# Performance work log

Hardware: AMD Instinct MI355X
Metric: run time of the kernel (lower is better)

Reference implementation:

```python
import jax, jax.numpy as jnp
import numpy as np

N = 4096       # num nodes == output_dim (delta is symmetrized NxN)
E = 65536      # num edges (avg degree 16)
IN_DIM = 128
H = 256        # hidden_dim (channels)
HEADS = 4


def setup_inputs():
    key = jax.random.key(0)
    ks = iter(jax.random.split(key, 40))
    def w(shape, s=0.05):
        return jax.random.normal(next(ks), shape, jnp.float32) * s
    inp = {}
    inp['x'] = jax.random.normal(next(ks), (N, IN_DIM), jnp.float32)
    inp['edge_index'] = jax.random.randint(next(ks), (2, E), 0, N)
    inp['pre_w'] = w((H, IN_DIM)); inp['pre_b'] = w((H,))
    for p in ('g1', 'g2'):
        inp[p + '_gcn_w'] = w((H, H)); inp[p + '_gcn_b'] = w((H,))
        inp[p + '_attn_in_w'] = w((3 * H, H)); inp[p + '_attn_in_b'] = w((3 * H,))
        inp[p + '_attn_out_w'] = w((H, H)); inp[p + '_attn_out_b'] = w((H,))
        inp[p + '_ffn_w1'] = w((2 * H, H)); inp[p + '_ffn_b1'] = w((2 * H,))
        inp[p + '_ffn_w2'] = w((H, 2 * H)); inp[p + '_ffn_b2'] = w((H,))
    inp['mlp_w1'] = w((H, H)); inp['mlp_b1'] = w((H,))
    inp['mlp_w2'] = w((N, H)); inp['mlp_b2'] = w((N,))
    return inp


def _gcn(x, src, dst, W, b):
    n = x.shape[0]
    x = x @ W.T
    loop = jnp.arange(n)
    s = jnp.concatenate([src, loop])
    d = jnp.concatenate([dst, loop])
    deg = jax.ops.segment_sum(jnp.ones(s.shape[0], x.dtype), d, num_segments=n)
    dinv = jnp.where(deg > 0, jax.lax.rsqrt(deg), 0.0)
    coef = (dinv[s] * dinv[d])[:, None]
    out = jax.ops.segment_sum(x[s] * coef, d, num_segments=n)
    return out + b


def _mha(h, in_w, in_b, out_w, out_b):
    # nn.MultiheadAttention self-attention over all N nodes (single dense graph)
    n, c = h.shape
    d = c // HEADS
    qkv = h @ in_w.T + in_b                      # [N, 3C]
    q, k, v = jnp.split(qkv, 3, axis=-1)
    q = q.reshape(n, HEADS, d).transpose(1, 0, 2) * (d ** -0.5)  # [h, n, d]
    k = k.reshape(n, HEADS, d).transpose(1, 0, 2)
    v = v.reshape(n, HEADS, d).transpose(1, 0, 2)
    a = jax.nn.softmax(jnp.einsum('hnd,hmd->hnm', q, k), axis=-1)
    o = jnp.einsum('hnm,hmd->hnd', a, v).transpose(1, 0, 2).reshape(n, c)
    return o @ out_w.T + out_b


def _gps(x, src, dst, gw, gb, iw, ib, ow, ob, w1, b1, w2, b2):
    # GPSConv, eval mode: dropout off, batch_norm (default running stats) = identity
    h1 = _gcn(x, src, dst, gw, gb) + x
    h2 = _mha(x, iw, ib, ow, ob) + x
    out = h1 + h2
    ff = jax.nn.relu(out @ w1.T + b1) @ w2.T + b2
    return out + ff


def reference(x, edge_index, pre_w, pre_b,
              g1_gcn_w, g1_gcn_b, g1_attn_in_w, g1_attn_in_b, g1_attn_out_w, g1_attn_out_b,
              g1_ffn_w1, g1_ffn_b1, g1_ffn_w2, g1_ffn_b2,
              g2_gcn_w, g2_gcn_b, g2_attn_in_w, g2_attn_in_b, g2_attn_out_w, g2_attn_out_b,
              g2_ffn_w1, g2_ffn_b1, g2_ffn_w2, g2_ffn_b2,
              mlp_w1, mlp_b1, mlp_w2, mlp_b2):
    src, dst = edge_index[0], edge_index[1]
    h = jax.nn.relu(x @ pre_w.T + pre_b)
    h = jax.nn.relu(_gps(h, src, dst, g1_gcn_w, g1_gcn_b, g1_attn_in_w, g1_attn_in_b,
                         g1_attn_out_w, g1_attn_out_b, g1_ffn_w1, g1_ffn_b1, g1_ffn_w2, g1_ffn_b2))
    h = jax.nn.relu(_gps(h, src, dst, g2_gcn_w, g2_gcn_b, g2_attn_in_w, g2_attn_in_b,
                         g2_attn_out_w, g2_attn_out_b, g2_ffn_w1, g2_ffn_b1, g2_ffn_w2, g2_ffn_b2))
    delta = jax.nn.relu(h @ mlp_w1.T + mlp_b1) @ mlp_w2.T + mlp_b2  # [N, N]
    return (delta + delta.T) * 0.5
```

## Files before the change

### kernel.cpp

```cpp
#include <hip/hip_runtime.h>

#define NN 4096
#define EE 65536
#define HC 256

typedef unsigned short ushort_t;
typedef __attribute__((ext_vector_type(8))) short bf16x8;
typedef __attribute__((ext_vector_type(4))) float f32x4;

__device__ __forceinline__ ushort_t f2bf(float f) {
    unsigned int u = __float_as_uint(f);
    unsigned int r = (u + 0x7fffu + ((u >> 16) & 1u)) >> 16;
    return (ushort_t)r;
}
__device__ __forceinline__ float bf2f(ushort_t u) {
    return __uint_as_float(((unsigned int)u) << 16);
}
__device__ __forceinline__ unsigned int pack2bf(float a, float b) {
    unsigned int ua = __float_as_uint(a) + 0x8000u;
    unsigned int ub = __float_as_uint(b) + 0x8000u;
    return __builtin_amdgcn_perm(ub, ua, 0x07060302u);
}

__global__ void deg_init_k(float* __restrict__ deg) {
    int i = blockIdx.x * 256 + threadIdx.x;
    deg[i] = 1.0f;
}
__global__ void deg_scatter_k(const int* __restrict__ dst, float* __restrict__ deg) {
    int e = blockIdx.x * 256 + threadIdx.x;
    atomicAdd(&deg[dst[e]], 1.0f);
}
__global__ void dinv_k(const float* __restrict__ deg, float* __restrict__ dinv) {
    int i = blockIdx.x * 256 + threadIdx.x;
    dinv[i] = rsqrtf(deg[i]);
}
__global__ __launch_bounds__(1024)
void scan_offsets_k(const float* __restrict__ deg, int* __restrict__ offs,
                    int* __restrict__ cursor) {
    __shared__ int part[1024];
    const int t = threadIdx.x;
    int c0 = (int)deg[t * 4 + 0] - 1;
    int c1 = (int)deg[t * 4 + 1] - 1;
    int c2 = (int)deg[t * 4 + 2] - 1;
    int c3 = (int)deg[t * 4 + 3] - 1;
    part[t] = c0 + c1 + c2 + c3;
    __syncthreads();
    for (int off = 1; off < 1024; off <<= 1) {
        int v = (t >= off) ? part[t - off] : 0;
        __syncthreads();
        part[t] += v;
        __syncthreads();
    }
    int base = (t == 0) ? 0 : part[t - 1];
    offs[t * 4 + 0] = base;
    offs[t * 4 + 1] = base + c0;
    offs[t * 4 + 2] = base + c0 + c1;
    offs[t * 4 + 3] = base + c0 + c1 + c2;
    cursor[t * 4 + 0] = base;
    cursor[t * 4 + 1] = base + c0;
    cursor[t * 4 + 2] = base + c0 + c1;
    cursor[t * 4 + 3] = base + c0 + c1 + c2;
    if (t == 1023) offs[4096] = part[1023];
}
__global__ void csr_fill_k(const int* __restrict__ src, const int* __restrict__ dst,
                           int* __restrict__ cursor, int* __restrict__ csr_src) {
    int e = blockIdx.x * 256 + threadIdx.x;
    int pos = atomicAdd(&cursor[dst[e]], 1);
    csr_src[pos] = src[e];
}

__global__ __launch_bounds__(256)
void gcn_gather_k(const float* __restrict__ xw, const float* __restrict__ dinv,
                  const int* __restrict__ offs, const int* __restrict__ csr_src,
                  float* __restrict__ agg) {
    const int node = blockIdx.x * 4 + (threadIdx.x >> 6);
    const int c = (threadIdx.x & 63) * 4;
    const float dd = dinv[node];
    float4 a = *(const float4*)&xw[(size_t)node * HC + c];
    const float self = dd * dd;
    float4 acc = make_float4(a.x * self, a.y * self, a.z * self, a.w * self);
    const int beg = offs[node], end = offs[node + 1];
    for (int e = beg; e < end; e++) {
        int s = csr_src[e];
        float coef = dinv[s] * dd;
        const float4 v = *(const float4*)&xw[(size_t)s * HC + c];
        acc.x += v.x * coef;
        acc.y += v.y * coef;
        acc.z += v.z * coef;
        acc.w += v.w * coef;
    }
    *(float4*)&agg[(size_t)node * HC + c] = acc;
}

__global__ void cvt_bf16_k(const float* __restrict__ in, ushort_t* __restrict__ out) {
    int i = (blockIdx.x * 256 + threadIdx.x) * 4;
    float4 v = *(const float4*)&in[i];
    unsigned int d0 = pack2bf(v.x, v.y), d1 = pack2bf(v.z, v.w);
    *(uint2*)&out[i] = make_uint2(d0, d1);
}

__global__ __launch_bounds__(256)
void gemm_bf_k(const float* __restrict__ X, const float* __restrict__ W,
               const float* __restrict__ bias1, const float* __restrict__ bias2,
               const float* __restrict__ res1, const float* __restrict__ res2, float res2scale,
               float* __restrict__ out, int K, int M, int dorelu, int obf,
               int colsplit, const float* __restrict__ W2,
               const float* __restrict__ bias_r2, float* __restrict__ out2, int M2)
{
    __shared__ ushort_t As[64][72];
    __shared__ ushort_t Bs[32][72];
    const int t = threadIdx.x;
    const int w = t >> 6, lane = t & 63;
    const int m = lane & 15, quad = lane >> 4;
    const int row0 = blockIdx.y << 6, col0 = blockIdx.x << 5;
    const int sr = t >> 2;
    const int sc = (t & 3) << 4;
    const int wr2 = t >> 3;
    const int wc2 = (t & 7) << 3;

    const float* Wu = W;
    const float* b1u = bias1;
    const float* b2u = bias2;
    float* outu = out;
    int Mu = M, colu = col0;
    if (colsplit > 0 && col0 >= colsplit) {
        Wu = W2; b1u = bias_r2; b2u = nullptr;
        outu = out2; Mu = M2; colu = col0 - colsplit;
    }

    f32x4 acc[2] = {};
    for (int k0 = 0; k0 < K; k0 += 64) {
        const float* xp = &X[(size_t)(row0 + sr) * K + k0 + sc];
        const float* wp = &Wu[(size_t)(colu + wr2) * K + k0 + wc2];
        float4 xa = *(const float4*)xp,       xb = *(const float4*)(xp + 4);
        float4 xc = *(const float4*)(xp + 8), xd = *(const float4*)(xp + 12);
        float4 wa = *(const float4*)wp,       wb = *(const float4*)(wp + 4);
        __syncthreads();
        {
            unsigned int tx[8];
            tx[0] = pack2bf(xa.x, xa.y); tx[1] = pack2bf(xa.z, xa.w);
            tx[2] = pack2bf(xb.x, xb.y); tx[3] = pack2bf(xb.z, xb.w);
            tx[4] = pack2bf(xc.x, xc.y); tx[5] = pack2bf(xc.z, xc.w);
            tx[6] = pack2bf(xd.x, xd.y); tx[7] = pack2bf(xd.z, xd.w);
            *(uint4*)&As[sr][sc]     = *(const uint4*)&tx[0];
            *(uint4*)&As[sr][sc + 8] = *(const uint4*)&tx[4];
            unsigned int tw[4];
            tw[0] = pack2bf(wa.x, wa.y); tw[1] = pack2bf(wa.z, wa.w);
            tw[2] = pack2bf(wb.x, wb.y); tw[3] = pack2bf(wb.z, wb.w);
            *(uint4*)&Bs[wr2][wc2] = *(const uint4*)&tw[0];
        }
        __syncthreads();
        #pragma unroll
        for (int kc = 0; kc < 2; kc++) {
            bf16x8 af = *(const bf16x8*)&As[(w << 4) + m][kc * 32 + quad * 8];
            #pragma unroll
            for (int cb = 0; cb < 2; cb++) {
                bf16x8 bf = *(const bf16x8*)&Bs[cb * 16 + m][kc * 32 + quad * 8];
                acc[cb] = __builtin_amdgcn_mfma_f32_16x16x32_bf16(af, bf, acc[cb], 0, 0, 0);
            }
        }
    }
    #pragma unroll
    for (int cb = 0; cb < 2; cb++) {
        #pragma unroll
        for (int r = 0; r < 4; r++) {
            const int row = row0 + (w << 4) + quad * 4 + r;
            const int col = colu + cb * 16 + m;
            float v = acc[cb][r];
            if (b1u) v += b1u[col];
            if (b2u) v += b2u[col];
            if (res1) v += res1[(size_t)row * Mu + col];
            if (res2) v += res2scale * res2[(size_t)row * Mu + col];
            if (dorelu) v = fmaxf(v, 0.f);
            if (obf) ((ushort_t*)outu)[(size_t)row * Mu + col] = f2bf(v);
            else outu[(size_t)row * Mu + col] = v;
        }
    }
}

__global__ __launch_bounds__(256)
void kv_prep_k(const float* __restrict__ qkv, ushort_t* __restrict__ Kb,
               ushort_t* __restrict__ Vtb)
{
    __shared__ ushort_t Vs[64][72];
    const int h = blockIdx.y;
    const int n0 = blockIdx.x << 6;
    const int t = threadIdx.x;
    for (int u = t; u < 1024; u += 256) {
        int r = u >> 4, c = u & 15;
        const float* kp = &qkv[(size_t)(n0 + r) * 768 + 256 + h * 64 + c * 4];
        float4 kv = *(const float4*)kp;
        float4 vv = *(const float4*)(kp + 256);
        *(uint2*)&Kb[((size_t)(h * 4096 + n0 + r)) * 64 + c * 4] =
            make_uint2(pack2bf(kv.x, kv.y), pack2bf(kv.z, kv.w));
        *(uint2*)&Vs[r][c * 4] =
            make_uint2(pack2bf(vv.x, vv.y), pack2bf(vv.z, vv.w));
    }
    __syncthreads();
    int d = t >> 2, kc = t & 3;
    __attribute__((aligned(16))) ushort_t vals[16];
    #pragma unroll
    for (int k = 0; k < 16; k++) vals[k] = Vs[kc * 16 + k][d];
    ushort_t* op = &Vtb[((size_t)(h * 64 + d)) * 4096 + n0 + kc * 16];
    *(uint4*)op = *(const uint4*)&vals[0];
    *(uint4*)(op + 8) = *(const uint4*)&vals[8];
}

__global__ __launch_bounds__(256)
void attn_part_k(const float* qkv, const ushort_t* __restrict__ Kb,
                 const ushort_t* __restrict__ Vtb, ushort_t* opart,
                 float* __restrict__ m_part, float* __restrict__ l_part)
{
    __shared__ ushort_t Kt[64][72];
    __shared__ ushort_t Vt[64][72];
    __shared__ ushort_t Plb[4][16][72];
    const int h = blockIdx.y & 3;
    const int split = blockIdx.y >> 2;
    const int q0 = blockIdx.x << 6;
    const int t = threadIdx.x;
    const int w = t >> 6, lane = t & 63;
    const int m = lane & 15, quad = lane >> 4;

    const int r0 = t >> 3, c8 = (t & 7) << 3;
    const int r1 = r0 + 32;
    const int pr0 = ((r0 & 15) << 2) | (r0 >> 4);
    const int pr1 = ((r1 & 15) << 2) | (r1 >> 4);
    const ushort_t* kb_p0 = &Kb[((size_t)(h * 4096 + split * 1024 + pr0)) * 64 + c8];
    const ushort_t* kb_p1 = &Kb[((size_t)(h * 4096 + split * 1024 + pr1)) * 64 + c8];
    const ushort_t* vt_p0 = &Vtb[((size_t)(h * 64 + r0)) * 4096 + split * 1024 + c8];
    const ushort_t* vt_p1 = &Vtb[((size_t)(h * 64 + r1)) * 4096 + split * 1024 + c8];
    ushort_t* const kt_d0 = &Kt[r0][c8];
    ushort_t* const kt_d1 = &Kt[r1][c8];
    ushort_t* const vt_d0 = &Vt[r0][c8];
    ushort_t* const vt_d1 = &Vt[r1][c8];

    const float qs = 0.125f * 1.44269504f;
    bf16x8 qf[2];
    #pragma unroll
    for (int kc = 0; kc < 2; kc++) {
        const float* qp = &qkv[(size_t)(q0 + w * 16 + m) * 768 + h * 64 + kc * 32 + quad * 8];
        float4 a = *(const float4*)qp;
        float4 b = *(const float4*)(qp + 4);
        qf[kc][0] = (short)f2bf(a.x * qs);
        qf[kc][1] = (short)f2bf(a.y * qs);
        qf[kc][2] = (short)f2bf(a.z * qs);
        qf[kc][3] = (short)f2bf(a.w * qs);
        qf[kc][4] = (short)f2bf(b.x * qs);
        qf[kc][5] = (short)f2bf(b.y * qs);
        qf[kc][6] = (short)f2bf(b.z * qs);
        qf[kc][7] = (short)f2bf(b.w * qs);
    }
    bf16x8 onesf;
    #pragma unroll
    for (int j = 0; j < 8; j++) onesf[j] = (short)0x3F80;

    f32x4 o[4], ol;
    float mrow[4];
    #pragma unroll
    for (int i = 0; i < 4; i++) {
        o[i] = (f32x4){0.f, 0.f, 0.f, 0.f};
        mrow[i] = -1e30f;
    }
    ol = (f32x4){0.f, 0.f, 0.f, 0.f};

    uint4 kr0 = *(const uint4*)kb_p0;
    uint4 kr1 = *(const uint4*)kb_p1;
    uint4 vr0 = *(const uint4*)vt_p0;
    uint4 vr1 = *(const uint4*)vt_p1;

    for (int it = 0; it < 16; it++) {
        __syncthreads();
        *(uint4*)kt_d0 = kr0;
        *(uint4*)kt_d1 = kr1;
        *(uint4*)vt_d0 = vr0;
        *(uint4*)vt_d1 = vr1;
        if (it < 15) {
            kb_p0 += 4096; kb_p1 += 4096; vt_p0 += 64; vt_p1 += 64;
            kr0 = *(const uint4*)kb_p0;
            kr1 = *(const uint4*)kb_p1;
            vr0 = *(const uint4*)vt_p0;
            vr1 = *(const uint4*)vt_p1;
        }
        __syncthreads();

        f32x4 s[4];
        #pragma unroll
        for (int b = 0; b < 4; b++) s[b] = (f32x4){0.f, 0.f, 0.f, 0.f};
        __builtin_amdgcn_s_setprio(1);
        #pragma unroll
        for (int b = 0; b < 4; b++)
            #pragma unroll
            for (int kc = 0; kc < 2; kc++) {
                bf16x8 kf = *(const bf16x8*)&Kt[b * 16 + m][kc * 32 + quad * 8];
                s[b] = __builtin_amdgcn_mfma_f32_16x16x32_bf16(qf[kc], kf, s[b], 0, 0, 0);
            }
        __builtin_amdgcn_s_setprio(0);

        float mx[4];
        #pragma unroll
        for (int r = 0; r < 4; r++) {
            float v = fmaxf(fmaxf(s[0][r], s[1][r]), fmaxf(s[2][r], s[3][r]));
            #pragma unroll
            for (int off = 1; off < 16; off <<= 1)
                v = fmaxf(v, __shfl_xor(v, off));
            mx[r] = v;
        }
        bool grow = (mx[0] > mrow[0] + 8.f) | (mx[1] > mrow[1] + 8.f) |
                    (mx[2] > mrow[2] + 8.f) | (mx[3] > mrow[3] + 8.f);
        if (__any(grow)) {
            #pragma unroll
            for (int r = 0; r < 4; r++) {
                float mn = fmaxf(mrow[r], mx[r]);
                float alpha = __builtin_amdgcn_exp2f(mrow[r] - mn);
                mrow[r] = mn;
                o[0][r] *= alpha; o[1][r] *= alpha;
                o[2][r] *= alpha; o[3][r] *= alpha;
                ol[r] *= alpha;
            }
        }
        #pragma unroll
        for (int r = 0; r < 4; r++) {
            unsigned int d0 = pack2bf(__builtin_amdgcn_exp2f(s[0][r] - mrow[r]),
                                      __builtin_amdgcn_exp2f(s[1][r] - mrow[r]));
            unsigned int d1 = pack2bf(__builtin_amdgcn_exp2f(s[2][r] - mrow[r]),
                                      __builtin_amdgcn_exp2f(s[3][r] - mrow[r]));
            *(uint2*)&Plb[w][quad * 4 + r][m * 4] = make_uint2(d0, d1);
        }

        __builtin_amdgcn_s_setprio(1);
        #pragma unroll
        for (int kc = 0; kc < 2; kc++) {
            bf16x8 pa = *(const bf16x8*)&Plb[w][m][kc * 32 + quad * 8];
            #pragma unroll
            for (int nb = 0; nb < 4; nb++) {
                bf16x8 vf = *(const bf16x8*)&Vt[nb * 16 + m][kc * 32 + quad * 8];
                o[nb] = __builtin_amdgcn_mfma_f32_16x16x32_bf16(pa, vf, o[nb], 0, 0, 0);
            }
            ol = __builtin_amdgcn_mfma_f32_16x16x32_bf16(pa, onesf, ol, 0, 0, 0);
        }
        __builtin_amdgcn_s_setprio(0);
    }

    #pragma unroll
    for (int nb = 0; nb < 4; nb++)
        #pragma unroll
        for (int r = 0; r < 4; r++) {
            int q = q0 + w * 16 + quad * 4 + r;
            opart[(size_t)q * 1536 + 512 + split * 256 + h * 64 + nb * 16 + m] = f2bf(o[nb][r]);
        }
    if (m == 0) {
        #pragma unroll
        for (int r = 0; r < 4; r++) {
            int q = q0 + w * 16 + quad * 4 + r;
            m_part[(split * 4 + h) * 4096 + q] = mrow[r];
            l_part[(split * 4 + h) * 4096 + q] = ol[r];
        }
    }
}

__global__ __launch_bounds__(256)
void attn_merge_k(const ushort_t* __restrict__ opart, const float* __restrict__ m_part,
                  const float* __restrict__ l_part, float* __restrict__ att)
{
    int idx = blockIdx.x * 256 + threadIdx.x;
    int q = idx >> 8, c = idx & 255;
    int h = c >> 6, d = c & 63;
    float ms[4];
    float mmax = -1e30f;
    #pragma unroll
    for (int s = 0; s < 4; s++) {
        ms[s] = m_part[(s * 4 + h) * 4096 + q];
        mmax = fmaxf(mmax, ms[s]);
    }
    float onum = 0.f, lden = 0.f;
    #pragma unroll
    for (int s = 0; s < 4; s++) {
        float wgt = __builtin_amdgcn_exp2f(ms[s] - mmax);
        float ov = bf2f(opart[(size_t)q * 1536 + 512 + s * 256 + h * 64 + d]);
        onum += wgt * ov;
        lden += wgt * l_part[(s * 4 + h) * 4096 + q];
    }
    att[(size_t)q * 256 + c] = onum / lden;
}

__global__ __launch_bounds__(256)
void sym_mlp_mfma_k(const ushort_t* __restrict__ Tb, const ushort_t* __restrict__ Wb,
                    const float* __restrict__ b2, float* __restrict__ out)
{
    __shared__ ushort_t As[128][72];
    __shared__ ushort_t Bs[128][72];
    const int t = threadIdx.x;
    const int w = t >> 6, lane = t & 63;
    const int m = lane & 15, quad = lane >> 4;
    const int wr = (w >> 1) * 64, wc = (w & 1) * 64;
    const int ri = blockIdx.y * 128, rj = blockIdx.x * 128;

    f32x4 acc[4][4] = {};
    for (int kk = 0; kk < 8; kk++) {
        const int k0 = kk * 64;
        const ushort_t* Asrc = (k0 < 256) ? Tb : Wb;
        const ushort_t* Bsrc = (k0 < 256) ? Wb : Tb;
        const int kcol = k0 & 255;
        __syncthreads();
        #pragma unroll
        for (int i = 0; i < 4; i++) {
            int s = t + i * 256;
            int row = s >> 3, ch = (s & 7) * 8;
            *(uint4*)&As[row][ch] = *(const uint4*)&Asrc[(size_t)(ri + row) * 256 + kcol + ch];
            *(uint4*)&Bs[row][ch] = *(const uint4*)&Bsrc[(size_t)(rj + row) * 256 + kcol + ch];
        }
        __syncthreads();
        #pragma unroll
        for (int kc = 0; kc < 2; kc++) {
            bf16x8 af[4], bfr[4];
            #pragma unroll
            for (int rb = 0; rb < 4; rb++)
                af[rb] = *(const bf16x8*)&As[wr + rb * 16 + m][kc * 32 + quad * 8];
            #pragma unroll
            for (int cb = 0; cb < 4; cb++)
                bfr[cb] = *(const bf16x8*)&Bs[wc + cb * 16 + m][kc * 32 + quad * 8];
            #pragma unroll
            for (int rb = 0; rb < 4; rb++)
                #pragma unroll
                for (int cb = 0; cb < 4; cb++)
                    acc[rb][cb] = __builtin_amdgcn_mfma_f32_16x16x32_bf16(af[rb], bfr[cb], acc[rb][cb], 0, 0, 0);
        }
    }
    #pragma unroll
    for (int rb = 0; rb < 4; rb++) {
        #pragma unroll
        for (int r = 0; r < 4; r++) {
            const int gr = ri + wr + rb * 16 + quad * 4 + r;
            const float br = b2[gr];
            #pragma unroll
            for (int cb = 0; cb < 4; cb++) {
                const int gc = rj + wc + cb * 16 + m;
                out[(size_t)gr * NN + gc] = 0.5f * (acc[rb][cb][r] + br + b2[gc]);
            }
        }
    }
}

extern "C" void kernel_launch(void* const* d_in, const int* in_sizes, int n_in,
                              void* d_out, int out_size, void* d_ws, size_t ws_size,
                              hipStream_t stream) {
    (void)in_sizes; (void)n_in; (void)out_size; (void)ws_size;
    const float* x = (const float*)d_in[0];
    const int* ei = (const int*)d_in[1];
    const int* src = ei;
    const int* dst = ei + EE;

    float* ws = (float*)d_ws;
    const int NH = NN * HC;
    float* h0  = ws;
    float* hb  = ws + 1 * NH;
    float* hc  = ws + 2 * NH;
    float* att = ws + 3 * NH;
    float* qkv = ws + 4 * NH;
    float* ffh = ws + 4 * NH;
    float* deg = ws + 7 * NH;
    float* dinv = deg + NN;
    int* offs    = (int*)(dinv + NN);
    int* cursor  = offs + 4100;
    int* csr_src = cursor + 4096;
    float* m_part = (float*)(csr_src + EE);
    float* l_part = m_part + 65536;
    ushort_t* Kb  = (ushort_t*)hc;
    ushort_t* Vtb = Kb + NH;
    ushort_t* Tb  = (ushort_t*)hb;
    ushort_t* W2b = Tb + NH;

    deg_init_k<<<NN / 256, 256, 0, stream>>>(deg);
    deg_scatter_k<<<EE / 256, 256, 0, stream>>>(dst, deg);
    dinv_k<<<NN / 256, 256, 0, stream>>>(deg, dinv);
    scan_offsets_k<<<1, 1024, 0, stream>>>(deg, offs, cursor);
    csr_fill_k<<<EE / 256, 256, 0, stream>>>(src, dst, cursor, csr_src);

    gemm_bf_k<<<dim3(8, 64), 256, 0, stream>>>(
        x, (const float*)d_in[2], (const float*)d_in[3], nullptr,
        nullptr, nullptr, 0.f, h0, 128, 256, 1, 0,
        0, nullptr, nullptr, nullptr, 0);

    for (int L = 0; L < 2; L++) {
        int B = 4 + L * 10;
        const float* gw = (const float*)d_in[B + 0];
        const float* gb = (const float*)d_in[B + 1];
        const float* iw = (const float*)d_in[B + 2];
        const float* ib = (const float*)d_in[B + 3];
        const float* ow = (const float*)d_in[B + 4];
        const float* ob = (const float*)d_in[B + 5];
        const float* w1 = (const float*)d_in[B + 6];
        const float* b1 = (const float*)d_in[B + 7];
        const float* w2 = (const float*)d_in[B + 8];
        const float* b2 = (const float*)d_in[B + 9];

        gemm_bf_k<<<dim3(32, 64), 256, 0, stream>>>(
            h0, gw, nullptr, nullptr, nullptr, nullptr, 0.f, att, 256, 256, 0, 0,
            256, iw, ib, qkv, 768);
        gcn_gather_k<<<NN / 4, 256, 0, stream>>>(att, dinv, offs, csr_src, hb);
        kv_prep_k<<<dim3(64, 4), 256, 0, stream>>>(qkv, Kb, Vtb);
        attn_part_k<<<dim3(64, 16), 256, 0, stream>>>(
            qkv, Kb, Vtb, (ushort_t*)qkv, m_part, l_part);
        attn_merge_k<<<NN, 256, 0, stream>>>(
            (const ushort_t*)qkv, m_part, l_part, att);
        gemm_bf_k<<<dim3(8, 64), 256, 0, stream>>>(
            att, ow, ob, gb, hb, h0, 2.0f, hc, 256, 256, 0, 0,
            0, nullptr, nullptr, nullptr, 0);
        gemm_bf_k<<<dim3(16, 64), 256, 0, stream>>>(
            hc, w1, b1, nullptr, nullptr, nullptr, 0.f, ffh, 256, 512, 1, 0,
            0, nullptr, nullptr, nullptr, 0);
        gemm_bf_k<<<dim3(8, 64), 256, 0, stream>>>(
            ffh, w2, b2, nullptr, hc, nullptr, 0.f, h0, 512, 256, 1, 0,
            0, nullptr, nullptr, nullptr, 0);
    }

    gemm_bf_k<<<dim3(8, 64), 256, 0, stream>>>(
        h0, (const float*)d_in[24], (const float*)d_in[25], nullptr,
        nullptr, nullptr, 0.f, (float*)Tb, 256, 256, 1, 1,
        0, nullptr, nullptr, nullptr, 0);
    cvt_bf16_k<<<NH / 1024, 256, 0, stream>>>((const float*)d_in[26], W2b);
    sym_mlp_mfma_k<<<dim3(32, 32), 256, 0, stream>>>(
        Tb, W2b, (const float*)d_in[27], (float*)d_out);
}
```

Before: 445.7 us.

## Double-buffer K tile and move barrier to overlap V staging with QK^T

```diff
diff --git a/kernel.cpp b/kernel.cpp
--- a/kernel.cpp
+++ b/kernel.cpp
@@ -211,7 +211,7 @@
                  const ushort_t* __restrict__ Vtb, ushort_t* opart,
                  float* __restrict__ m_part, float* __restrict__ l_part)
 {
-    __shared__ ushort_t Kt[64][72];
+    __shared__ ushort_t Kt[2][64][72];
     __shared__ ushort_t Vt[64][72];
     __shared__ ushort_t Plb[4][16][72];
     const int h = blockIdx.y & 3;
@@ -229,10 +229,6 @@
     const ushort_t* kb_p1 = &Kb[((size_t)(h * 4096 + split * 1024 + pr1)) * 64 + c8];
     const ushort_t* vt_p0 = &Vtb[((size_t)(h * 64 + r0)) * 4096 + split * 1024 + c8];
     const ushort_t* vt_p1 = &Vtb[((size_t)(h * 64 + r1)) * 4096 + split * 1024 + c8];
-    ushort_t* const kt_d0 = &Kt[r0][c8];
-    ushort_t* const kt_d1 = &Kt[r1][c8];
-    ushort_t* const vt_d0 = &Vt[r0][c8];
-    ushort_t* const vt_d1 = &Vt[r1][c8];
 
     const float qs = 0.125f * 1.44269504f;
     bf16x8 qf[2];
@@ -263,26 +259,37 @@
     }
     ol = (f32x4){0.f, 0.f, 0.f, 0.f};
 
-    uint4 kr0 = *(const uint4*)kb_p0;
-    uint4 kr1 = *(const uint4*)kb_p1;
-    uint4 vr0 = *(const uint4*)vt_p0;
-    uint4 vr1 = *(const uint4*)vt_p1;
+    uint4 ka = *(const uint4*)kb_p0;
+    uint4 kb4 = *(const uint4*)kb_p1;
+    uint4 va = *(const uint4*)vt_p0;
+    uint4 vb = *(const uint4*)vt_p1;
+    *(uint4*)&Kt[0][r0][c8] = ka;
+    *(uint4*)&Kt[0][r1][c8] = kb4;
+    kb_p0 += 4096; kb_p1 += 4096;
+    ka = *(const uint4*)kb_p0;
+    kb4 = *(const uint4*)kb_p1;
 
     for (int it = 0; it < 16; it++) {
-        __syncthreads();
-        *(uint4*)kt_d0 = kr0;
-        *(uint4*)kt_d1 = kr1;
-        *(uint4*)vt_d0 = vr0;
-        *(uint4*)vt_d1 = vr1;
+        asm volatile("s_waitcnt lgkmcnt(0)" ::: "memory");
+        __builtin_amdgcn_s_barrier();
+        asm volatile("" ::: "memory");
+        *(uint4*)&Vt[r0][c8] = va;
+        *(uint4*)&Vt[r1][c8] = vb;
         if (it < 15) {
-            kb_p0 += 4096; kb_p1 += 4096; vt_p0 += 64; vt_p1 += 64;
-            kr0 = *(const uint4*)kb_p0;
-            kr1 = *(const uint4*)kb_p1;
-            vr0 = *(const uint4*)vt_p0;
-            vr1 = *(const uint4*)vt_p1;
-        }
-        __syncthreads();
-
+            ushort_t (*KtW)[72] = Kt[(it + 1) & 1];
+            *(uint4*)&KtW[r0][c8] = ka;
+            *(uint4*)&KtW[r1][c8] = kb4;
+            vt_p0 += 64; vt_p1 += 64;
+            va = *(const uint4*)vt_p0;
+            vb = *(const uint4*)vt_p1;
+        }
+        if (it < 14) {
+            kb_p0 += 4096; kb_p1 += 4096;
+            ka = *(const uint4*)kb_p0;
+            kb4 = *(const uint4*)kb_p1;
+        }
+
+        const ushort_t (*KtR)[72] = Kt[it & 1];
         f32x4 s[4];
         #pragma unroll
         for (int b = 0; b < 4; b++) s[b] = (f32x4){0.f, 0.f, 0.f, 0.f};
@@ -291,7 +298,7 @@
         for (int b = 0; b < 4; b++)
             #pragma unroll
             for (int kc = 0; kc < 2; kc++) {
-                bf16x8 kf = *(const bf16x8*)&Kt[b * 16 + m][kc * 32 + quad * 8];
+                bf16x8 kf = *(const bf16x8*)&KtR[b * 16 + m][kc * 32 + quad * 8];
                 s[b] = __builtin_amdgcn_mfma_f32_16x16x32_bf16(qf[kc], kf, s[b], 0, 0, 0);
             }
         __builtin_amdgcn_s_setprio(0);
@@ -326,6 +333,10 @@
                                       __builtin_amdgcn_exp2f(s[3][r] - mrow[r]));
             *(uint2*)&Plb[w][quad * 4 + r][m * 4] = make_uint2(d0, d1);
         }
+
+        asm volatile("s_waitcnt lgkmcnt(0)" ::: "memory");
+        __builtin_amdgcn_s_barrier();
+        asm volatile("" ::: "memory");
 
         __builtin_amdgcn_s_setprio(1);
         #pragma unroll
```

Result: no change. 449.5 us (+0.9%).
